# Kernel optimization log

Hardware: AMD Instinct MI355X
Metric: run time of the kernel (lower is better)

## Reference

```python
import jax, jax.numpy as jnp
import numpy as np

JITTER = 0.002  # original adds 0.001*I globally plus 0.001*I on each diagonal block


def setup_inputs() -> dict:
    key = jax.random.key(0)
    k1, k2, k3 = jax.random.split(key, 3)
    T, N, D, Z = 4, 1024, 64, 4
    x = jax.random.normal(k1, (T, N, D), dtype=jnp.float32)      # per-task features
    W = jax.random.normal(k2, (T, Z), dtype=jnp.float32)         # task-to-latent mixing weights
    theta = jax.random.uniform(k3, (Z, 2), dtype=jnp.float32)    # [amplitude, inv-lengthscale] per latent GP
    return {"x": x, "W": W, "theta": theta}


def reference(x, W, theta):
    # Faithful, fused version of MTGP.rbf_kernel_mo_hete with x2=None and equal
    # task lengths. cov[mi, nj] = sum_z W[task(mi),z] W[task(nj),z] * theta[z,0]
    #   * exp(-theta[z,1]/2 * ||X[mi]-X[nj]||^2)  + JITTER on the diagonal.
    T, N, D = x.shape
    Z = theta.shape[0]
    M = T * N
    X = x.reshape(M, D)
    sq = jnp.sum(X * X, axis=-1)                                  # [M]
    sqd = jnp.maximum(sq[:, None] + sq[None, :] - 2.0 * X @ X.T, 0.0)  # [M, M]
    Wexp = jnp.repeat(W, N, axis=0)                               # [M, Z] task weight per point
    cov = JITTER * jnp.eye(M, dtype=x.dtype)
    for z in range(Z):  # small fixed loop over latent GPs
        Kz = theta[z, 0] * jnp.exp(-0.5 * theta[z, 1] * sqd)      # [M, M]
        cov = cov + (Wexp[:, z][:, None] * Wexp[:, z][None, :]) * Kz
    return cov
```

## Files before the change

### kernel.cpp

```cpp
#include <hip/hip_runtime.h>


#define M_PTS 4096
#define DIM 64
#define JITTER_F 0.002f
#define NEG_HALF_LOG2E (-0.72134752044448170f)
#define NBLK 2080

typedef __attribute__((ext_vector_type(8))) short short8v;
typedef __attribute__((ext_vector_type(4))) float f32x4;

union FragU { short8v v; uint2 h[2]; };

__device__ __forceinline__ float fast_exp2(float x) {
#if defined(__has_builtin)
#if __has_builtin(__builtin_amdgcn_exp2f)
  return __builtin_amdgcn_exp2f(x);
#else
  return exp2f(x);
#endif
#else
  return exp2f(x);
#endif
}

__device__ __forceinline__ unsigned bfr(float x) {
  unsigned u = __float_as_uint(x);
  return (u + 0x7FFFu + ((u >> 16) & 1u)) >> 16;
}
__device__ __forceinline__ float bff(unsigned h) {
  return __uint_as_float(h << 16);
}

__global__ __launch_bounds__(256) void mtgp_prep(
    const float* __restrict__ X, unsigned short* __restrict__ Xhi,
    unsigned short* __restrict__ Xlo, float* __restrict__ sqn) {
  const int gtid = blockIdx.x * 256 + threadIdx.x;
  const int row = gtid >> 2, part = gtid & 3;
  const float4* xr = (const float4*)(X + (size_t)row * DIM + part * 16);
  unsigned* hp = (unsigned*)(Xhi + (size_t)row * DIM + part * 16);
  unsigned* lp = (unsigned*)(Xlo + (size_t)row * DIM + part * 16);
  float s = 0.0f;
#define CVT2(xa, xb, oidx) { \
    unsigned ha = bfr(xa), hb = bfr(xb); \
    hp[oidx] = ha | (hb << 16); \
    unsigned la = bfr((xa) - bff(ha)), lb = bfr((xb) - bff(hb)); \
    lp[oidx] = la | (lb << 16); \
    s = fmaf((xa), (xa), s); s = fmaf((xb), (xb), s); }
#pragma unroll
  for (int i = 0; i < 4; ++i) {
    float4 vv = xr[i];
    CVT2(vv.x, vv.y, 2 * i)
    CVT2(vv.z, vv.w, 2 * i + 1)
  }
#undef CVT2
  s += __shfl_xor(s, 1);
  s += __shfl_xor(s, 2);
  if (part == 0) sqn[row] = s;
}

__global__ __launch_bounds__(256, 5) void mtgp_main(
    const unsigned short* __restrict__ Xhi, const unsigned short* __restrict__ Xlo,
    const float* __restrict__ sqn, const float* __restrict__ W,
    const float* __restrict__ theta, float* __restrict__ out) {
  __shared__ unsigned short Ahi[64 * 64], Alo[64 * 64];
  __shared__ unsigned short Bhi[64 * 64], Blo[64 * 64];

  const int item = blockIdx.x;
  int u = (int)(64.5f - sqrtf(4160.25f - 2.0f * (float)item));
  if (u < 0) u = 0;
  if (u > 63) u = 63;
  while (u > 0 && u * (129 - u) / 2 > item) --u;
  while (u < 63 && (u + 1) * (128 - u) / 2 <= item) ++u;
  const int v = u + (item - u * (129 - u) / 2);
  const int grow0 = u << 6, gj0 = v << 6;

  const int tid = threadIdx.x;

#pragma unroll
  for (int cc = 0; cc < 2; ++cc) {
    const int n = cc * 256 + tid;
    const int row = n >> 3, sl = n & 7;
    const int lofs = row * 64 + ((sl ^ (row & 7)) << 3);
    const int ga = (grow0 + row) * DIM + sl * 8;
    const int gb = (gj0 + row) * DIM + sl * 8;
    *(uint4*)&Ahi[lofs] = *(const uint4*)&Xhi[ga];
    *(uint4*)&Alo[lofs] = *(const uint4*)&Xlo[ga];
    *(uint4*)&Bhi[lofs] = *(const uint4*)&Xhi[gb];
    *(uint4*)&Blo[lofs] = *(const uint4*)&Xlo[gb];
  }
  __syncthreads();

  const int wid = tid >> 6, lane = tid & 63;
  const int wr = (wid >> 1) << 5;
  const int wc = (wid & 1) << 5;
  const int r16 = lane & 15, kg = lane >> 4, kg4 = kg << 2;

  f32x4 acc[2][2];
#pragma unroll
  for (int p = 0; p < 2; ++p) { acc[p][0] = (f32x4)0.0f; acc[p][1] = (f32x4)0.0f; }

#define FRAG_LD(dst, PANEL, rr) { \
    const int rb = (rr) * 64, sw = (rr) & 7; \
    dst.h[0] = *(const uint2*)&PANEL[rb + ((sl1 ^ sw) << 3) + hof]; \
    dst.h[1] = *(const uint2*)&PANEL[rb + (((sl1 + 2) ^ sw) << 3) + hof]; }

#pragma unroll
  for (int k0 = 0; k0 < 2; ++k0) {
    const int sl1 = k0 * 4 + (kg >> 1);
    const int hof = (kg & 1) * 4;
    FragU ah[2], al[2], bh[2], bl[2];
#pragma unroll
    for (int p = 0; p < 2; ++p) {
      const int ra = wr + p * 16 + r16;
      const int rb2 = wc + p * 16 + r16;
      FRAG_LD(ah[p], Ahi, ra)
      FRAG_LD(al[p], Alo, ra)
      FRAG_LD(bh[p], Bhi, rb2)
      FRAG_LD(bl[p], Blo, rb2)
    }
#pragma unroll
    for (int p = 0; p < 2; ++p)
#pragma unroll
      for (int q = 0; q < 2; ++q) {
        acc[p][q] = __builtin_amdgcn_mfma_f32_16x16x32_bf16(ah[p].v, bh[q].v, acc[p][q], 0, 0, 0);
        acc[p][q] = __builtin_amdgcn_mfma_f32_16x16x32_bf16(ah[p].v, bl[q].v, acc[p][q], 0, 0, 0);
        acc[p][q] = __builtin_amdgcn_mfma_f32_16x16x32_bf16(al[p].v, bh[q].v, acc[p][q], 0, 0, 0);
      }
  }
#undef FRAG_LD

  const int ti = u >> 4, tj = v >> 4;
  float czv[4], ezv[4];
#pragma unroll
  for (int z = 0; z < 4; ++z) {
    czv[z] = W[ti * 4 + z] * W[tj * 4 + z] * theta[2 * z];
    ezv[z] = NEG_HALF_LOG2E * theta[2 * z + 1];
  }
  f32x4 sqr[2];
#pragma unroll
  for (int p = 0; p < 2; ++p) sqr[p] = *(const f32x4*)&sqn[grow0 + wr + p * 16 + kg4];
  float sqc[2];
#pragma unroll
  for (int q = 0; q < 2; ++q) sqc[q] = sqn[gj0 + wc + q * 16 + r16];

#pragma unroll
  for (int p = 0; p < 2; ++p)
#pragma unroll
    for (int q = 0; q < 2; ++q)
#pragma unroll
      for (int rr = 0; rr < 4; ++rr) {
        const float d = acc[p][q][rr];
        const float sd = fmaxf(fmaf(-2.0f, d, sqr[p][rr] + sqc[q]), 0.0f);
        float val = czv[0] * fast_exp2(ezv[0] * sd);
        val = fmaf(czv[1], fast_exp2(ezv[1] * sd), val);
        val = fmaf(czv[2], fast_exp2(ezv[2] * sd), val);
        val = fmaf(czv[3], fast_exp2(ezv[3] * sd), val);
        if (u == v && wr + p * 16 + kg4 + rr == wc + q * 16 + r16) val += JITTER_F;
        acc[p][q][rr] = val;
      }

#pragma unroll
  for (int p = 0; p < 2; ++p)
#pragma unroll
    for (int rr = 0; rr < 4; ++rr) {
      float* rp = out + (size_t)(grow0 + wr + p * 16 + kg4 + rr) * M_PTS + gj0 + wc + r16;
      rp[0] = acc[p][0][rr];
      rp[16] = acc[p][1][rr];
    }
  if (u != v) {
#pragma unroll
    for (int q = 0; q < 2; ++q)
#pragma unroll
      for (int p = 0; p < 2; ++p) {
        f32x4* tp = (f32x4*)(out + (size_t)(gj0 + wc + q * 16 + r16) * M_PTS + grow0 + wr + p * 16 + kg4);
        *tp = acc[p][q];
      }
  }
}

extern "C" void kernel_launch(void* const* d_in, const int* in_sizes, int n_in,
                              void* d_out, int out_size, void* d_ws, size_t ws_size,
                              hipStream_t stream) {
  const float* x     = (const float*)d_in[0];
  const float* W     = (const float*)d_in[1];
  const float* theta = (const float*)d_in[2];
  float* out = (float*)d_out;

  float* sqn = (float*)d_ws;
  unsigned short* Xhi = (unsigned short*)((char*)d_ws + 16384);
  unsigned short* Xlo = (unsigned short*)((char*)d_ws + 16384 + 524288);

  mtgp_prep<<<dim3(64), dim3(256), 0, stream>>>(x, Xhi, Xlo, sqn);
  mtgp_main<<<dim3(NBLK), dim3(256), 0, stream>>>(Xhi, Xlo, sqn, W, theta, out);
}
```

Baseline: 26.76 us.

## Fuse bf16 split prep into main kernel and widen fragment loads

Drops the separate prep kernel. Each block now reads fp32 rows directly, splits them into hi/lo bf16 panels in shared memory, and computes the row norms locally, sharing them through LDS. Fragment loads become single 128-bit LDS reads, which relies on a reordered k-mapping that is consistent on both the A and B sides. In exchange, every block redoes the conversion, reads twice as many bytes from global memory as with bf16, and adds two barriers, while saving a kernel launch and the workspace round trip.

```diff
diff --git a/kernel.cpp b/kernel.cpp
--- a/kernel.cpp
+++ b/kernel.cpp
@@ -10,7 +10,7 @@
 typedef __attribute__((ext_vector_type(8))) short short8v;
 typedef __attribute__((ext_vector_type(4))) float f32x4;
 
-union FragU { short8v v; uint2 h[2]; };
+union FragU { short8v v; uint4 u; };
 
 __device__ __forceinline__ float fast_exp2(float x) {
 #if defined(__has_builtin)
@@ -32,37 +32,11 @@
   return __uint_as_float(h << 16);
 }
 
-__global__ __launch_bounds__(256) void mtgp_prep(
-    const float* __restrict__ X, unsigned short* __restrict__ Xhi,
-    unsigned short* __restrict__ Xlo, float* __restrict__ sqn) {
-  const int gtid = blockIdx.x * 256 + threadIdx.x;
-  const int row = gtid >> 2, part = gtid & 3;
-  const float4* xr = (const float4*)(X + (size_t)row * DIM + part * 16);
-  unsigned* hp = (unsigned*)(Xhi + (size_t)row * DIM + part * 16);
-  unsigned* lp = (unsigned*)(Xlo + (size_t)row * DIM + part * 16);
-  float s = 0.0f;
-#define CVT2(xa, xb, oidx) { \
-    unsigned ha = bfr(xa), hb = bfr(xb); \
-    hp[oidx] = ha | (hb << 16); \
-    unsigned la = bfr((xa) - bff(ha)), lb = bfr((xb) - bff(hb)); \
-    lp[oidx] = la | (lb << 16); \
-    s = fmaf((xa), (xa), s); s = fmaf((xb), (xb), s); }
-#pragma unroll
-  for (int i = 0; i < 4; ++i) {
-    float4 vv = xr[i];
-    CVT2(vv.x, vv.y, 2 * i)
-    CVT2(vv.z, vv.w, 2 * i + 1)
-  }
-#undef CVT2
-  s += __shfl_xor(s, 1);
-  s += __shfl_xor(s, 2);
-  if (part == 0) sqn[row] = s;
-}
-
-__global__ __launch_bounds__(256, 5) void mtgp_main(
-    const unsigned short* __restrict__ Xhi, const unsigned short* __restrict__ Xlo,
-    const float* __restrict__ sqn, const float* __restrict__ W,
-    const float* __restrict__ theta, float* __restrict__ out) {
+__global__ __launch_bounds__(256, 5) void mtgp_fused(
+    const float* __restrict__ X,
+    const float* __restrict__ W,
+    const float* __restrict__ theta,
+    float* __restrict__ out) {
   __shared__ unsigned short Ahi[64 * 64], Alo[64 * 64];
   __shared__ unsigned short Bhi[64 * 64], Blo[64 * 64];
 
@@ -77,18 +51,38 @@
 
   const int tid = threadIdx.x;
 
+  const int half = tid & 1;
+  const int srow = (tid & 127) >> 1;
+  const bool isB = (tid >= 128);
+  const int gsrow = (isB ? gj0 : grow0) + srow;
+  const float4* xr = (const float4*)(X + (size_t)gsrow * DIM + half * 32);
+  unsigned short* Ph = isB ? Bhi : Ahi;
+  unsigned short* Pl = isB ? Blo : Alo;
+  float s = 0.0f;
 #pragma unroll
-  for (int cc = 0; cc < 2; ++cc) {
-    const int n = cc * 256 + tid;
-    const int row = n >> 3, sl = n & 7;
-    const int lofs = row * 64 + ((sl ^ (row & 7)) << 3);
-    const int ga = (grow0 + row) * DIM + sl * 8;
-    const int gb = (gj0 + row) * DIM + sl * 8;
-    *(uint4*)&Ahi[lofs] = *(const uint4*)&Xhi[ga];
-    *(uint4*)&Alo[lofs] = *(const uint4*)&Xlo[ga];
-    *(uint4*)&Bhi[lofs] = *(const uint4*)&Xhi[gb];
-    *(uint4*)&Blo[lofs] = *(const uint4*)&Xlo[gb];
+  for (int kgs = 0; kgs < 4; ++kgs) {
+    const float4 v0 = xr[kgs];
+    const float4 v1 = xr[kgs + 4];
+    s = fmaf(v0.x, v0.x, s); s = fmaf(v0.y, v0.y, s);
+    s = fmaf(v0.z, v0.z, s); s = fmaf(v0.w, v0.w, s);
+    s = fmaf(v1.x, v1.x, s); s = fmaf(v1.y, v1.y, s);
+    s = fmaf(v1.z, v1.z, s); s = fmaf(v1.w, v1.w, s);
+    const unsigned h0 = bfr(v0.x), h1 = bfr(v0.y), h2 = bfr(v0.z), h3 = bfr(v0.w);
+    const unsigned h4 = bfr(v1.x), h5 = bfr(v1.y), h6 = bfr(v1.z), h7 = bfr(v1.w);
+    uint4 hv = make_uint4(h0 | (h1 << 16), h2 | (h3 << 16),
+                          h4 | (h5 << 16), h6 | (h7 << 16));
+    const unsigned l0 = bfr(v0.x - bff(h0)), l1 = bfr(v0.y - bff(h1));
+    const unsigned l2 = bfr(v0.z - bff(h2)), l3 = bfr(v0.w - bff(h3));
+    const unsigned l4 = bfr(v1.x - bff(h4)), l5 = bfr(v1.y - bff(h5));
+    const unsigned l6 = bfr(v1.z - bff(h6)), l7 = bfr(v1.w - bff(h7));
+    uint4 lv = make_uint4(l0 | (l1 << 16), l2 | (l3 << 16),
+                          l4 | (l5 << 16), l6 | (l7 << 16));
+    const int f = (half << 2) + kgs;
+    const int lofs = srow * 64 + ((f ^ (srow & 7)) << 3);
+    *(uint4*)&Ph[lofs] = hv;
+    *(uint4*)&Pl[lofs] = lv;
   }
+  s += __shfl_xor(s, 1);
   __syncthreads();
 
   const int wid = tid >> 6, lane = tid & 63;
@@ -101,23 +95,20 @@
   for (int p = 0; p < 2; ++p) { acc[p][0] = (f32x4)0.0f; acc[p][1] = (f32x4)0.0f; }
 
 #define FRAG_LD(dst, PANEL, rr) { \
-    const int rb = (rr) * 64, sw = (rr) & 7; \
-    dst.h[0] = *(const uint2*)&PANEL[rb + ((sl1 ^ sw) << 3) + hof]; \
-    dst.h[1] = *(const uint2*)&PANEL[rb + (((sl1 + 2) ^ sw) << 3) + hof]; }
+    dst.u = *(const uint4*)&PANEL[(rr) * 64 + ((f0 ^ ((rr) & 7)) << 3)]; }
 
 #pragma unroll
   for (int k0 = 0; k0 < 2; ++k0) {
-    const int sl1 = k0 * 4 + (kg >> 1);
-    const int hof = (kg & 1) * 4;
+    const int f0 = (k0 << 2) + kg;
     FragU ah[2], al[2], bh[2], bl[2];
 #pragma unroll
     for (int p = 0; p < 2; ++p) {
       const int ra = wr + p * 16 + r16;
-      const int rb2 = wc + p * 16 + r16;
+      const int rb = wc + p * 16 + r16;
       FRAG_LD(ah[p], Ahi, ra)
       FRAG_LD(al[p], Alo, ra)
-      FRAG_LD(bh[p], Bhi, rb2)
-      FRAG_LD(bl[p], Blo, rb2)
+      FRAG_LD(bh[p], Bhi, rb)
+      FRAG_LD(bl[p], Blo, rb)
     }
 #pragma unroll
     for (int p = 0; p < 2; ++p)
@@ -130,6 +121,11 @@
   }
 #undef FRAG_LD
 
+  __syncthreads();
+  if (half == 0) ((float*)Ahi)[(isB ? 64 : 0) + srow] = s;
+  __syncthreads();
+  const float* nrm = (const float*)Ahi;
+
   const int ti = u >> 4, tj = v >> 4;
   float czv[4], ezv[4];
 #pragma unroll
@@ -139,10 +135,10 @@
   }
   f32x4 sqr[2];
 #pragma unroll
-  for (int p = 0; p < 2; ++p) sqr[p] = *(const f32x4*)&sqn[grow0 + wr + p * 16 + kg4];
+  for (int p = 0; p < 2; ++p) sqr[p] = *(const f32x4*)&nrm[wr + p * 16 + kg4];
   float sqc[2];
 #pragma unroll
-  for (int q = 0; q < 2; ++q) sqc[q] = sqn[gj0 + wc + q * 16 + r16];
+  for (int q = 0; q < 2; ++q) sqc[q] = nrm[64 + wc + q * 16 + r16];
 
 #pragma unroll
   for (int p = 0; p < 2; ++p)
@@ -187,10 +183,5 @@
   const float* theta = (const float*)d_in[2];
   float* out = (float*)d_out;
 
-  float* sqn = (float*)d_ws;
-  unsigned short* Xhi = (unsigned short*)((char*)d_ws + 16384);
-  unsigned short* Xlo = (unsigned short*)((char*)d_ws + 16384 + 524288);
-
-  mtgp_prep<<<dim3(64), dim3(256), 0, stream>>>(x, Xhi, Xlo, sqn);
-  mtgp_main<<<dim3(NBLK), dim3(256), 0, stream>>>(Xhi, Xlo, sqn, W, theta, out);
+  mtgp_fused<<<dim3(NBLK), dim3(256), 0, stream>>>(x, W, theta, out);
 }
```

Measured after the change: 24.29 us (median of 2 runs). -9.2%, faster.
